# Kernel tuning notes

Hardware: AMD Instinct MI355X
Metric: run time of the kernel (lower is better)

Reference implementation:

```python
import jax, jax.numpy as jnp
import numpy as np

NORM_SCALE = float(np.sqrt(1.0 / (128 * 4 * 4)))  # from module __init__
TEMP = 30.0
NORM_EPS = 1e-5


def setup_inputs() -> dict:
    key = jax.random.key(0)
    k1, k2, k3, k4, k5, k6 = jax.random.split(key, 6)
    b, n, c, h, w = 16, 4, 128, 32, 32
    return {
        "f_list1": jax.random.normal(k1, (b, n, c, h, w), dtype=jnp.float32),
        "f_list2": jax.random.normal(k2, (b, n, c, h, w), dtype=jnp.float32),
        "t_pos1": jax.random.normal(k3, (1, 1, c), dtype=jnp.float32),
        "t_pos2": jax.random.normal(k4, (1, 1, c), dtype=jnp.float32),
        "W_qk_w": jax.random.normal(k5, (32, c), dtype=jnp.float32) * (1.0 / np.sqrt(c)),
        "W_qk_b": jax.random.normal(k6, (32,), dtype=jnp.float32) * 0.01,
    }


def _l2_normalize(x, eps=1e-12):
    # torch F.normalize(p=2, dim=-1): x / max(||x||, eps)
    nrm = jnp.sqrt(jnp.sum(x * x, axis=-1, keepdims=True))
    return x / jnp.maximum(nrm, eps)


def reference(f_list1, f_list2, t_pos1, t_pos2, W_qk_w, W_qk_b):
    b, n, c, h, w = f_list1.shape
    hw = h * w
    # (b*n, hw, c) token-major layout + learned positional offsets
    f_l1 = f_list1.reshape(b * n, c, hw).transpose(0, 2, 1) + t_pos1
    f_l2 = f_list2.reshape(b * n, c, hw).transpose(0, 2, 1) + t_pos2
    # shared QK projection to head dim 32
    f_q = _l2_normalize(jnp.einsum('bsc,dc->bsd', f_l1, W_qk_w) + W_qk_b)
    f_k = _l2_normalize(jnp.einsum('bsc,dc->bsd', f_l2, W_qk_w) + W_qk_b)
    # cosine-similarity attention with fixed temperature 30
    attn = jax.nn.softmax(TEMP * jnp.einsum('bqd,bkd->bqk', f_q, f_k), axis=-1)
    f_r = jnp.einsum('bqk,bkc->bqc', attn, f_l2) + f_l2  # value = f_l2, plus residual
    f_r = f_r.transpose(0, 2, 1).reshape(b * n, c, h, w)
    # InstanceL2Norm (size_average=True): x * scale * sqrt(C*H*W / (sum(x^2) + eps)) per sample
    ssq = jnp.sum(f_r * f_r, axis=(1, 2, 3), keepdims=True)
    return f_r * (NORM_SCALE * jnp.sqrt((c * h * w) / (ssq + NORM_EPS)))
```

## Files before the change

### kernel.cpp

```cpp
#include <hip/hip_runtime.h>
#include <math.h>

typedef short s16x8 __attribute__((ext_vector_type(8)));
typedef float f32x4 __attribute__((ext_vector_type(4)));
typedef __bf16 bf16_t;
typedef bf16_t bf16x8 __attribute__((ext_vector_type(8)));
typedef bf16_t bf16x4 __attribute__((ext_vector_type(4)));

#define MFMA16 __builtin_amdgcn_mfma_f32_16x16x32_bf16
#define C_DIM 128
#define S_DIM 1024

__global__ __launch_bounds__(256) void k_wt(const float* __restrict__ Ww,
                                            float* __restrict__ Wt) {
    for (int e = threadIdx.x; e < 32 * C_DIM; e += 256) {
        int d = e >> 7, c = e & (C_DIM - 1);
        Wt[c * 32 + d] = Ww[e];
    }
}

__global__ __launch_bounds__(256) void k_v(const float* __restrict__ f2,
                                           const float* __restrict__ pos2,
                                           bf16_t* __restrict__ Vtb) {
    const int i = blockIdx.x * 256 + threadIdx.x;
    float4 v = ((const float4*)f2)[i];
    const float p = pos2[(i >> 8) & (C_DIM - 1)];
    bf16x4 o = {(bf16_t)(v.x + p), (bf16_t)(v.y + p),
                (bf16_t)(v.z + p), (bf16_t)(v.w + p)};
    *(bf16x4*)(Vtb + (size_t)i * 4) = o;
}

__global__ __launch_bounds__(256) void k_proj(
    const float* __restrict__ f1, const float* __restrict__ f2,
    const float* __restrict__ pos1, const float* __restrict__ pos2,
    const float* __restrict__ Wt, const float* __restrict__ Wb,
    bf16_t* __restrict__ fqb, bf16_t* __restrict__ fkb) {
    const int g = blockIdx.x * 256 + threadIdx.x;
    const int b = g >> 10;
    const int t = g & (S_DIM - 1);
    const float* x1 = f1 + (size_t)b * C_DIM * S_DIM + t;
    const float* x2 = f2 + (size_t)b * C_DIM * S_DIM + t;
    float q[32], k[32];
#pragma unroll
    for (int d = 0; d < 32; ++d) { q[d] = 0.f; k[d] = 0.f; }
#pragma unroll 4
    for (int c = 0; c < C_DIM; ++c) {
        float a1 = x1[(size_t)c * S_DIM] + pos1[c];
        float a2 = x2[(size_t)c * S_DIM] + pos2[c];
#pragma unroll
        for (int d = 0; d < 32; ++d) {
            float w = Wt[c * 32 + d];
            q[d] = fmaf(w, a1, q[d]);
            k[d] = fmaf(w, a2, k[d]);
        }
    }
    float sq = 0.f, sk = 0.f;
#pragma unroll
    for (int d = 0; d < 32; ++d) {
        q[d] += Wb[d]; k[d] += Wb[d];
        sq = fmaf(q[d], q[d], sq);
        sk = fmaf(k[d], k[d], sk);
    }
    const float rq = 30.0f / fmaxf(sqrtf(sq), 1e-12f);
    const float rk = 1.0f / fmaxf(sqrtf(sk), 1e-12f);
    bf16_t* oq = fqb + (size_t)g * 32;
    bf16_t* ok = fkb + (size_t)g * 32;
#pragma unroll
    for (int c8 = 0; c8 < 4; ++c8) {
        bf16x8 vq, vk;
#pragma unroll
        for (int j = 0; j < 8; ++j) {
            vq[j] = (bf16_t)(q[c8 * 8 + j] * rq);
            vk[j] = (bf16_t)(k[c8 * 8 + j] * rk);
        }
        *(bf16x8*)(oq + c8 * 8) = vq;
        *(bf16x8*)(ok + c8 * 8) = vk;
    }
}

__global__ __launch_bounds__(512) void k_attn(
    const bf16_t* __restrict__ fqb, const bf16_t* __restrict__ fkb,
    const bf16_t* __restrict__ Vtb, float* __restrict__ fr,
    float* __restrict__ ssq) {
    __shared__ __align__(16) bf16_t Ks[64][40];
    __shared__ __align__(16) bf16_t Vs[128][72];
    __shared__ __align__(16) bf16_t Ps[8][16][72];
    __shared__ float wred[8];

    const int tid = threadIdx.x;
    const int w = tid >> 6;
    const int lane = tid & 63;
    const int l15 = lane & 15;
    const int Q = lane >> 4;
    const int b = blockIdx.y;
    const int qw = blockIdx.x * 128 + w * 16;

    const s16x8 qa =
        *(const s16x8*)(fqb + ((size_t)b * S_DIM + qw + l15) * 32 + Q * 8);

    f32x4 acc[8];
    const f32x4 fz = {0.f, 0.f, 0.f, 0.f};
#pragma unroll
    for (int cg = 0; cg < 8; ++cg) acc[cg] = fz;
    float m[4] = {-1e30f, -1e30f, -1e30f, -1e30f};
    float lsum[4] = {0.f, 0.f, 0.f, 0.f};

    for (int kb = 0; kb < 16; ++kb) {
        const int k0 = kb * 64;
        __syncthreads();
        if (tid < 256) {
            int row = tid >> 2, c8 = (tid & 3) * 8;
            *(s16x8*)&Ks[row][c8] =
                *(const s16x8*)(fkb + ((size_t)b * S_DIM + k0 + row) * 32 + c8);
        }
#pragma unroll
        for (int it = 0; it < 2; ++it) {
            int e = it * 512 + tid;
            int row = e >> 3, c8 = (e & 7) * 8;
            *(s16x8*)&Vs[row][c8] =
                *(const s16x8*)(Vtb + ((size_t)b * C_DIM + row) * S_DIM + k0 + c8);
        }
        __syncthreads();

        f32x4 sc[4];
#pragma unroll
        for (int n = 0; n < 4; ++n) {
            s16x8 kf = *(const s16x8*)&Ks[l15 + 16 * n][Q * 8];
            sc[n] = MFMA16(qa, kf, fz, 0, 0, 0);
        }

        float corr[4];
#pragma unroll
        for (int s = 0; s < 4; ++s) {
            float mx = fmaxf(fmaxf(sc[0][s], sc[1][s]), fmaxf(sc[2][s], sc[3][s]));
            mx = fmaxf(mx, __shfl_xor(mx, 1, 16));
            mx = fmaxf(mx, __shfl_xor(mx, 2, 16));
            mx = fmaxf(mx, __shfl_xor(mx, 4, 16));
            mx = fmaxf(mx, __shfl_xor(mx, 8, 16));
            float mn = fmaxf(m[s], mx);
            corr[s] = __expf(m[s] - mn);
            float sum = 0.f;
#pragma unroll
            for (int n = 0; n < 4; ++n) {
                float p = __expf(sc[n][s] - mn);
                sum += p;
                Ps[w][4 * Q + s][l15 + 16 * n] = (bf16_t)p;
            }
            sum += __shfl_xor(sum, 1, 16);
            sum += __shfl_xor(sum, 2, 16);
            sum += __shfl_xor(sum, 4, 16);
            sum += __shfl_xor(sum, 8, 16);
            lsum[s] = lsum[s] * corr[s] + sum;
            m[s] = mn;
        }
        {
            const int src = (l15 >> 2) << 4;
            float t0 = __shfl(corr[0], src);
            float t1 = __shfl(corr[1], src);
            float t2 = __shfl(corr[2], src);
            float t3 = __shfl(corr[3], src);
            const int rs = l15 & 3;
            const float cq = rs == 0 ? t0 : rs == 1 ? t1 : rs == 2 ? t2 : t3;
#pragma unroll
            for (int cg = 0; cg < 8; ++cg) {
                acc[cg][0] *= cq; acc[cg][1] *= cq;
                acc[cg][2] *= cq; acc[cg][3] *= cq;
            }
        }

#pragma unroll
        for (int h = 0; h < 2; ++h) {
            s16x8 pb = *(const s16x8*)&Ps[w][l15][h * 32 + Q * 8];
#pragma unroll
            for (int cg = 0; cg < 8; ++cg) {
                s16x8 va = *(const s16x8*)&Vs[16 * cg + l15][h * 32 + Q * 8];
                acc[cg] = MFMA16(va, pb, acc[cg], 0, 0, 0);
            }
        }
    }

    float invq;
    {
        const int src = (l15 >> 2) << 4;
        float t0 = __shfl(lsum[0], src);
        float t1 = __shfl(lsum[1], src);
        float t2 = __shfl(lsum[2], src);
        float t3 = __shfl(lsum[3], src);
        const int rs = l15 & 3;
        invq = 1.0f / (rs == 0 ? t0 : rs == 1 ? t1 : rs == 2 ? t2 : t3);
    }

    float sp = 0.f;
#pragma unroll
    for (int cg = 0; cg < 8; ++cg) {
#pragma unroll
        for (int s = 0; s < 4; ++s) {
            const int c = 16 * cg + 4 * Q + s;
            const size_t idx = ((size_t)b * C_DIM + c) * S_DIM + qw + l15;
            float val = acc[cg][s] * invq + (float)Vtb[idx];
            fr[idx] = val;
            sp = fmaf(val, val, sp);
        }
    }
    sp += __shfl_down(sp, 32);
    sp += __shfl_down(sp, 16);
    sp += __shfl_down(sp, 8);
    sp += __shfl_down(sp, 4);
    sp += __shfl_down(sp, 2);
    sp += __shfl_down(sp, 1);
    if (lane == 0) wred[w] = sp;
    __syncthreads();
    if (tid == 0) {
        float s = 0.f;
#pragma unroll
        for (int i = 0; i < 8; ++i) s += wred[i];
        atomicAdd(&ssq[b], s);
    }
}

__global__ __launch_bounds__(256) void k_out(float* __restrict__ fr,
                                             const float* __restrict__ ssq) {
    const int b = blockIdx.x >> 5;
    const float scale =
        0.022097086912079608f * sqrtf(131072.0f / (ssq[b] + 1e-5f));
    float4* p = (float4*)fr + (size_t)blockIdx.x * 1024;
#pragma unroll
    for (int it = 0; it < 4; ++it) {
        float4 v = p[it * 256 + threadIdx.x];
        v.x *= scale; v.y *= scale; v.z *= scale; v.w *= scale;
        p[it * 256 + threadIdx.x] = v;
    }
}

extern "C" void kernel_launch(void* const* d_in, const int* in_sizes, int n_in,
                              void* d_out, int out_size, void* d_ws,
                              size_t ws_size, hipStream_t stream) {
    const float* f1 = (const float*)d_in[0];
    const float* f2 = (const float*)d_in[1];
    const float* pos1 = (const float*)d_in[2];
    const float* pos2 = (const float*)d_in[3];
    const float* Ww = (const float*)d_in[4];
    const float* Wb = (const float*)d_in[5];
    float* out = (float*)d_out;

    bf16_t* fqb = (bf16_t*)d_ws;
    bf16_t* fkb = fqb + 2097152;
    bf16_t* Vtb = fkb + 2097152;
    float* Wt = (float*)((char*)d_ws + 25165824);
    float* ssq = (float*)((char*)d_ws + 25182208);

    k_wt<<<1, 256, 0, stream>>>(Ww, Wt);
    k_v<<<8192, 256, 0, stream>>>(f2, pos2, Vtb);
    k_proj<<<256, 256, 0, stream>>>(f1, f2, pos1, pos2, Wt, Wb, fqb, fkb);
    hipMemsetAsync(ssq, 0, 256, stream);
    k_attn<<<dim3(8, 64), 512, 0, stream>>>(fqb, fkb, Vtb, out, ssq);
    k_out<<<2048, 256, 0, stream>>>(out, ssq);
}
```

Before: 225.4 us.

## Fuse V conversion into projection, keep softmax probs in registers, lazy rescale

The separate k_v kernel is removed. The projection kernel now stages f1/f2 tiles through LDS with vectorized loads and also writes the bf16 V tensor. The attention kernel swaps MFMA operands so each lane holds full score columns. Probabilities are redistributed with shuffles instead of a shared Ps buffer, and the per-row max rescale is skipped unless the max grows by more than 8, with blocks shrunk to 256 threads. This cuts a kernel launch, one HBM read of f2, LDS traffic and rescale work, at the cost of extra shuffles and less K/V tile reuse per block.

After: 221.1 us. Within noise of the previous version (-1.9%).

```diff
diff --git a/kernel.cpp b/kernel.cpp
--- a/kernel.cpp
+++ b/kernel.cpp
@@ -4,7 +4,6 @@
 typedef short s16x8 __attribute__((ext_vector_type(8)));
 typedef float f32x4 __attribute__((ext_vector_type(4)));
 typedef __bf16 bf16_t;
-typedef bf16_t bf16x8 __attribute__((ext_vector_type(8)));
 typedef bf16_t bf16x4 __attribute__((ext_vector_type(4)));
 
 #define MFMA16 __builtin_amdgcn_mfma_f32_16x16x32_bf16
@@ -19,41 +18,55 @@
     }
 }
 
-__global__ __launch_bounds__(256) void k_v(const float* __restrict__ f2,
-                                           const float* __restrict__ pos2,
-                                           bf16_t* __restrict__ Vtb) {
-    const int i = blockIdx.x * 256 + threadIdx.x;
-    float4 v = ((const float4*)f2)[i];
-    const float p = pos2[(i >> 8) & (C_DIM - 1)];
-    bf16x4 o = {(bf16_t)(v.x + p), (bf16_t)(v.y + p),
-                (bf16_t)(v.z + p), (bf16_t)(v.w + p)};
-    *(bf16x4*)(Vtb + (size_t)i * 4) = o;
-}
-
 __global__ __launch_bounds__(256) void k_proj(
     const float* __restrict__ f1, const float* __restrict__ f2,
     const float* __restrict__ pos1, const float* __restrict__ pos2,
     const float* __restrict__ Wt, const float* __restrict__ Wb,
-    bf16_t* __restrict__ fqb, bf16_t* __restrict__ fkb) {
-    const int g = blockIdx.x * 256 + threadIdx.x;
-    const int b = g >> 10;
-    const int t = g & (S_DIM - 1);
-    const float* x1 = f1 + (size_t)b * C_DIM * S_DIM + t;
-    const float* x2 = f2 + (size_t)b * C_DIM * S_DIM + t;
+    bf16_t* __restrict__ fqb, bf16_t* __restrict__ fkb,
+    bf16_t* __restrict__ Vtb) {
+    __shared__ float LX1[16][260];
+    __shared__ float LX2[16][260];
+    const int tid = threadIdx.x;
+    const int b = blockIdx.x >> 2;
+    const int t0 = (blockIdx.x & 3) * 256;
+
     float q[32], k[32];
 #pragma unroll
     for (int d = 0; d < 32; ++d) { q[d] = 0.f; k[d] = 0.f; }
+
+    for (int cc = 0; cc < C_DIM; cc += 16) {
+        __syncthreads();
+#pragma unroll
+        for (int it = 0; it < 4; ++it) {
+            const int e4 = it * 256 + tid;
+            const int r = e4 >> 6, t4 = (e4 & 63) << 2;
+            const int c = cc + r;
+            const size_t base = ((size_t)b * C_DIM + c) * S_DIM + t0 + t4;
+            const float p1 = pos1[c], p2 = pos2[c];
+            float4 v1 = *(const float4*)(f1 + base);
+            float4 v2 = *(const float4*)(f2 + base);
+            v1.x += p1; v1.y += p1; v1.z += p1; v1.w += p1;
+            v2.x += p2; v2.y += p2; v2.z += p2; v2.w += p2;
+            *(float4*)&LX1[r][t4] = v1;
+            *(float4*)&LX2[r][t4] = v2;
+            bf16x4 vb = {(bf16_t)v2.x, (bf16_t)v2.y, (bf16_t)v2.z, (bf16_t)v2.w};
+            *(bf16x4*)(Vtb + base) = vb;
+        }
+        __syncthreads();
 #pragma unroll 4
-    for (int c = 0; c < C_DIM; ++c) {
-        float a1 = x1[(size_t)c * S_DIM] + pos1[c];
-        float a2 = x2[(size_t)c * S_DIM] + pos2[c];
-#pragma unroll
-        for (int d = 0; d < 32; ++d) {
-            float w = Wt[c * 32 + d];
-            q[d] = fmaf(w, a1, q[d]);
-            k[d] = fmaf(w, a2, k[d]);
-        }
-    }
+        for (int r = 0; r < 16; ++r) {
+            const float a1 = LX1[r][tid];
+            const float a2 = LX2[r][tid];
+            const float* wrow = Wt + (cc + r) * 32;
+#pragma unroll
+            for (int d = 0; d < 32; ++d) {
+                const float wv = wrow[d];
+                q[d] = fmaf(wv, a1, q[d]);
+                k[d] = fmaf(wv, a2, k[d]);
+            }
+        }
+    }
+
     float sq = 0.f, sk = 0.f;
 #pragma unroll
     for (int d = 0; d < 32; ++d) {
@@ -63,29 +76,33 @@
     }
     const float rq = 30.0f / fmaxf(sqrtf(sq), 1e-12f);
     const float rk = 1.0f / fmaxf(sqrtf(sk), 1e-12f);
-    bf16_t* oq = fqb + (size_t)g * 32;
-    bf16_t* ok = fkb + (size_t)g * 32;
-#pragma unroll
-    for (int c8 = 0; c8 < 4; ++c8) {
-        bf16x8 vq, vk;
-#pragma unroll
-        for (int j = 0; j < 8; ++j) {
-            vq[j] = (bf16_t)(q[c8 * 8 + j] * rq);
-            vk[j] = (bf16_t)(k[c8 * 8 + j] * rk);
-        }
-        *(bf16x8*)(oq + c8 * 8) = vq;
-        *(bf16x8*)(ok + c8 * 8) = vk;
-    }
-}
-
-__global__ __launch_bounds__(512) void k_attn(
+    const size_t g = (size_t)b * S_DIM + t0 + tid;
+    bf16_t* oq = fqb + g * 32;
+    bf16_t* ok = fkb + g * 32;
+#pragma unroll
+    for (int c4 = 0; c4 < 8; ++c4) {
+        bf16x4 vq = {(bf16_t)(q[c4 * 4] * rq), (bf16_t)(q[c4 * 4 + 1] * rq),
+                     (bf16_t)(q[c4 * 4 + 2] * rq), (bf16_t)(q[c4 * 4 + 3] * rq)};
+        bf16x4 vk = {(bf16_t)(k[c4 * 4] * rk), (bf16_t)(k[c4 * 4 + 1] * rk),
+                     (bf16_t)(k[c4 * 4 + 2] * rk), (bf16_t)(k[c4 * 4 + 3] * rk)};
+        *(bf16x4*)(oq + c4 * 4) = vq;
+        *(bf16x4*)(ok + c4 * 4) = vk;
+    }
+}
+
+static __device__ __forceinline__ unsigned int pkbf(float a, float b) {
+    union { bf16_t h[2]; unsigned int u; } z;
+    z.h[0] = (bf16_t)a; z.h[1] = (bf16_t)b;
+    return z.u;
+}
+
+__global__ __launch_bounds__(256) void k_attn(
     const bf16_t* __restrict__ fqb, const bf16_t* __restrict__ fkb,
     const bf16_t* __restrict__ Vtb, float* __restrict__ fr,
     float* __restrict__ ssq) {
     __shared__ __align__(16) bf16_t Ks[64][40];
     __shared__ __align__(16) bf16_t Vs[128][72];
-    __shared__ __align__(16) bf16_t Ps[8][16][72];
-    __shared__ float wred[8];
+    __shared__ float wred[4];
 
     const int tid = threadIdx.x;
     const int w = tid >> 6;
@@ -93,7 +110,7 @@
     const int l15 = lane & 15;
     const int Q = lane >> 4;
     const int b = blockIdx.y;
-    const int qw = blockIdx.x * 128 + w * 16;
+    const int qw = blockIdx.x * 64 + w * 16;
 
     const s16x8 qa =
         *(const s16x8*)(fqb + ((size_t)b * S_DIM + qw + l15) * 32 + Q * 8);
@@ -102,21 +119,22 @@
     const f32x4 fz = {0.f, 0.f, 0.f, 0.f};
 #pragma unroll
     for (int cg = 0; cg < 8; ++cg) acc[cg] = fz;
-    float m[4] = {-1e30f, -1e30f, -1e30f, -1e30f};
-    float lsum[4] = {0.f, 0.f, 0.f, 0.f};
+    float m = -1e30f, l = 0.f;
+    const int srcbase = l15 + 32 * (Q & 1);
+    const int nsel = Q >> 1;
 
     for (int kb = 0; kb < 16; ++kb) {
         const int k0 = kb * 64;
         __syncthreads();
-        if (tid < 256) {
-            int row = tid >> 2, c8 = (tid & 3) * 8;
+        {
+            const int row = tid >> 2, c8 = (tid & 3) * 8;
             *(s16x8*)&Ks[row][c8] =
                 *(const s16x8*)(fkb + ((size_t)b * S_DIM + k0 + row) * 32 + c8);
         }
 #pragma unroll
-        for (int it = 0; it < 2; ++it) {
-            int e = it * 512 + tid;
-            int row = e >> 3, c8 = (e & 7) * 8;
+        for (int it = 0; it < 4; ++it) {
+            const int e = it * 256 + tid;
+            const int row = e >> 3, c8 = (e & 7) * 8;
             *(s16x8*)&Vs[row][c8] =
                 *(const s16x8*)(Vtb + ((size_t)b * C_DIM + row) * S_DIM + k0 + c8);
         }
@@ -125,70 +143,70 @@
         f32x4 sc[4];
 #pragma unroll
         for (int n = 0; n < 4; ++n) {
-            s16x8 kf = *(const s16x8*)&Ks[l15 + 16 * n][Q * 8];
-            sc[n] = MFMA16(qa, kf, fz, 0, 0, 0);
-        }
-
-        float corr[4];
-#pragma unroll
-        for (int s = 0; s < 4; ++s) {
-            float mx = fmaxf(fmaxf(sc[0][s], sc[1][s]), fmaxf(sc[2][s], sc[3][s]));
-            mx = fmaxf(mx, __shfl_xor(mx, 1, 16));
-            mx = fmaxf(mx, __shfl_xor(mx, 2, 16));
-            mx = fmaxf(mx, __shfl_xor(mx, 4, 16));
-            mx = fmaxf(mx, __shfl_xor(mx, 8, 16));
-            float mn = fmaxf(m[s], mx);
-            corr[s] = __expf(m[s] - mn);
-            float sum = 0.f;
-#pragma unroll
-            for (int n = 0; n < 4; ++n) {
-                float p = __expf(sc[n][s] - mn);
-                sum += p;
-                Ps[w][4 * Q + s][l15 + 16 * n] = (bf16_t)p;
-            }
-            sum += __shfl_xor(sum, 1, 16);
-            sum += __shfl_xor(sum, 2, 16);
-            sum += __shfl_xor(sum, 4, 16);
-            sum += __shfl_xor(sum, 8, 16);
-            lsum[s] = lsum[s] * corr[s] + sum;
-            m[s] = mn;
-        }
-        {
-            const int src = (l15 >> 2) << 4;
-            float t0 = __shfl(corr[0], src);
-            float t1 = __shfl(corr[1], src);
-            float t2 = __shfl(corr[2], src);
-            float t3 = __shfl(corr[3], src);
-            const int rs = l15 & 3;
-            const float cq = rs == 0 ? t0 : rs == 1 ? t1 : rs == 2 ? t2 : t3;
+            const s16x8 kf = *(const s16x8*)&Ks[l15 + 16 * n][Q * 8];
+            sc[n] = MFMA16(kf, qa, fz, 0, 0, 0);
+        }
+
+        float mx = sc[0][0];
+#pragma unroll
+        for (int n = 0; n < 4; ++n)
+#pragma unroll
+            for (int s = 0; s < 4; ++s) mx = fmaxf(mx, sc[n][s]);
+        mx = fmaxf(mx, __shfl_xor(mx, 16));
+        mx = fmaxf(mx, __shfl_xor(mx, 32));
+
+        if (!__all(mx <= m + 8.0f)) {
+            const float mn = fmaxf(m, mx);
+            const float corr = __expf(m - mn);
 #pragma unroll
             for (int cg = 0; cg < 8; ++cg) {
-                acc[cg][0] *= cq; acc[cg][1] *= cq;
-                acc[cg][2] *= cq; acc[cg][3] *= cq;
-            }
+                acc[cg][0] *= corr; acc[cg][1] *= corr;
+                acc[cg][2] *= corr; acc[cg][3] *= corr;
+            }
+            l *= corr; m = mn;
+        }
+
+        float pv[4][4];
+        float sum = 0.f;
+#pragma unroll
+        for (int n = 0; n < 4; ++n)
+#pragma unroll
+            for (int s = 0; s < 4; ++s) {
+                pv[n][s] = __expf(sc[n][s] - m);
+                sum += pv[n][s];
+            }
+        sum += __shfl_xor(sum, 16);
+        sum += __shfl_xor(sum, 32);
+        l += sum;
+
+        unsigned int wpk[4][2];
+#pragma unroll
+        for (int n = 0; n < 4; ++n) {
+            wpk[n][0] = pkbf(pv[n][0], pv[n][1]);
+            wpk[n][1] = pkbf(pv[n][2], pv[n][3]);
         }
 
 #pragma unroll
         for (int h = 0; h < 2; ++h) {
-            s16x8 pb = *(const s16x8*)&Ps[w][l15][h * 32 + Q * 8];
+            union { unsigned int u[4]; s16x8 v; } pb;
+#pragma unroll
+            for (int half = 0; half < 2; ++half)
+#pragma unroll
+                for (int a = 0; a < 2; ++a) {
+                    const int src = srcbase + 16 * half;
+                    const unsigned int g0 = __shfl((int)wpk[2 * h][a], src);
+                    const unsigned int g1 = __shfl((int)wpk[2 * h + 1][a], src);
+                    pb.u[half * 2 + a] = nsel ? g1 : g0;
+                }
 #pragma unroll
             for (int cg = 0; cg < 8; ++cg) {
-                s16x8 va = *(const s16x8*)&Vs[16 * cg + l15][h * 32 + Q * 8];
-                acc[cg] = MFMA16(va, pb, acc[cg], 0, 0, 0);
-            }
-        }
-    }
-
-    float invq;
-    {
-        const int src = (l15 >> 2) << 4;
-        float t0 = __shfl(lsum[0], src);
-        float t1 = __shfl(lsum[1], src);
-        float t2 = __shfl(lsum[2], src);
-        float t3 = __shfl(lsum[3], src);
-        const int rs = l15 & 3;
-        invq = 1.0f / (rs == 0 ? t0 : rs == 1 ? t1 : rs == 2 ? t2 : t3);
-    }
+                const s16x8 va = *(const s16x8*)&Vs[16 * cg + l15][h * 32 + Q * 8];
+                acc[cg] = MFMA16(va, pb.v, acc[cg], 0, 0, 0);
+            }
+        }
+    }
+
+    const float invq = 1.0f / l;
 
     float sp = 0.f;
 #pragma unroll
@@ -197,7 +215,7 @@
         for (int s = 0; s < 4; ++s) {
             const int c = 16 * cg + 4 * Q + s;
             const size_t idx = ((size_t)b * C_DIM + c) * S_DIM + qw + l15;
-            float val = acc[cg][s] * invq + (float)Vtb[idx];
+            const float val = acc[cg][s] * invq + (float)Vtb[idx];
             fr[idx] = val;
             sp = fmaf(val, val, sp);
         }
@@ -210,12 +228,8 @@
     sp += __shfl_down(sp, 1);
     if (lane == 0) wred[w] = sp;
     __syncthreads();
-    if (tid == 0) {
-        float s = 0.f;
-#pragma unroll
-        for (int i = 0; i < 8; ++i) s += wred[i];
-        atomicAdd(&ssq[b], s);
-    }
+    if (tid == 0)
+        atomicAdd(&ssq[b], wred[0] + wred[1] + wred[2] + wred[3]);
 }
 
 __global__ __launch_bounds__(256) void k_out(float* __restrict__ fr,
@@ -250,9 +264,8 @@
     float* ssq = (float*)((char*)d_ws + 25182208);
 
     k_wt<<<1, 256, 0, stream>>>(Ww, Wt);
-    k_v<<<8192, 256, 0, stream>>>(f2, pos2, Vtb);
-    k_proj<<<256, 256, 0, stream>>>(f1, f2, pos1, pos2, Wt, Wb, fqb, fkb);
+    k_proj<<<256, 256, 0, stream>>>(f1, f2, pos1, pos2, Wt, Wb, fqb, fkb, Vtb);
     hipMemsetAsync(ssq, 0, 256, stream);
-    k_attn<<<dim3(8, 64), 512, 0, stream>>>(fqb, fkb, Vtb, out, ssq);
+    k_attn<<<dim3(16, 64), 256, 0, stream>>>(fqb, fkb, Vtb, out, ssq);
     k_out<<<2048, 256, 0, stream>>>(out, ssq);
 }
```
